# Kernel tuning notes

Measured on AMD Instinct MI355X. Metric: run time of the kernel, lower is better.

Reference implementation:

```python
import jax, jax.numpy as jnp
import numpy as np

TOP_K = 2


def _mlp(x, w1, b1, w2, b2):
    # Linear -> GELU -> Linear (assumed MLP body)
    h = jax.nn.gelu(jnp.einsum('bsd,di->bsi', x, w1) + b1)
    return jnp.einsum('bsi,id->bsd', h, w2) + b2


def setup_inputs() -> dict:
    key = jax.random.key(0)
    ks = jax.random.split(key, 8)
    B, S, D, I, E = 2, 2048, 1024, 4096, 8
    s_in = 1.0 / np.sqrt(D)
    s_mid = 1.0 / np.sqrt(I)
    return {
        'x': jax.random.normal(ks[0], (B, S, D), jnp.float32),
        'gate_w': jax.random.normal(ks[1], (D, E), jnp.float32) * s_in,
        'gate_b': jnp.zeros((E,), jnp.float32),
        'sh_w1': jax.random.normal(ks[2], (D, I), jnp.float32) * s_in,
        'sh_b1': jnp.zeros((I,), jnp.float32),
        'sh_w2': jax.random.normal(ks[3], (I, D), jnp.float32) * s_mid,
        'sh_b2': jnp.zeros((D,), jnp.float32),
        'ew1': jax.random.normal(ks[4], (E, D, I), jnp.float32) * s_in,
        'eb1': jnp.zeros((E, I), jnp.float32),
        'ew2': jax.random.normal(ks[5], (E, I, D), jnp.float32) * s_mid,
        'eb2': jnp.zeros((E, D), jnp.float32),
    }


def reference(x, gate_w, gate_b, sh_w1, sh_b1, sh_w2, sh_b2, ew1, eb1, ew2, eb2):
    E = ew1.shape[0]
    # Router
    router_probs = jax.nn.softmax(jnp.einsum('bsd,de->bse', x, gate_w) + gate_b, axis=-1)
    expert_values, expert_indices = jax.lax.top_k(router_probs, k=TOP_K)  # (B,S,K)
    expert_values = expert_values / (jnp.sum(expert_values, axis=-1, keepdims=True) + 1e-9)
    # Dense compute of all experts (faithful to original)
    h = jax.nn.gelu(jnp.einsum('bsd,edi->bsei', x, ew1) + eb1)  # (B,S,E,I)
    all_outputs = jnp.einsum('bsei,eid->bsed', h, ew2) + eb2    # (B,S,E,D)
    # Combine: scatter top-k weights to dense (B,S,E) then weighted sum
    one_hot = jax.nn.one_hot(expert_indices, E, dtype=x.dtype)  # (B,S,K,E)
    weights_E = (one_hot * expert_values[..., None]).sum(axis=2)  # (B,S,E)
    moe_out = jnp.einsum('bse,bsed->bsd', weights_E, all_outputs)
    return x + _mlp(x, sh_w1, sh_b1, sh_w2, sh_b2) + moe_out
```

## Files before the change

kernel.cpp:

```cpp
#include <hip/hip_runtime.h>
#include <hip/hip_bf16.h>
#include <stdint.h>

typedef short bf16x8 __attribute__((ext_vector_type(8)));
typedef float f32x4  __attribute__((ext_vector_type(4)));
typedef unsigned short u16;

#define T_TOK 4096
#define D_DIM 1024
#define I_DIM 4096
#define NE    9
#define BK    32

__device__ __forceinline__ u16 f2bf(float f) {
    union { float f; uint32_t u; } v; v.f = f;
    uint32_t u = v.u;
    u += 0x7FFFu + ((u >> 16) & 1u);
    return (u16)(u >> 16);
}

__device__ __forceinline__ float gelu_fast(float v) {
    float c2 = 1.5957691216057308f * (v + 0.044715f * v * v * v);
    return v / (1.0f + __expf(-c2));
}

__device__ __forceinline__ void gl16(const void* g, void* l) {
    __builtin_amdgcn_global_load_lds(
        (const __attribute__((address_space(1))) void*)g,
        (__attribute__((address_space(3))) void*)l, 16, 0, 0);
}

#define DSR(dst, adr, IMM) \
    asm volatile("ds_read_b128 %0, %1 offset:" #IMM : "=v"(dst) : "v"(adr) : "memory")
#define WAIT_VM(N)   asm volatile("s_waitcnt vmcnt(" #N ")" ::: "memory")
#define WAIT_LG(N)   asm volatile("s_waitcnt lgkmcnt(" #N ")" ::: "memory")

__global__ void k_init(int* counts) {
    int i = threadIdx.x;
    if (i < 16) counts[i] = (i == 8) ? T_TOK : 0;
}

__global__ __launch_bounds__(256) void k_router(
    const float* __restrict__ x, const float* __restrict__ gw,
    const float* __restrict__ gb,
    int* counts, int* lists, int* tok_e, int* tok_pos, float* tok_w,
    u16* __restrict__ xb)
{
    int wave = threadIdx.x >> 6, lane = threadIdx.x & 63;
    int t = blockIdx.x * 4 + wave;
    const float* xr = x + (size_t)t * D_DIM;
    u16* xbr = xb + (size_t)t * D_DIM;

    float a[8];
#pragma unroll
    for (int e = 0; e < 8; ++e) a[e] = 0.f;
#pragma unroll
    for (int j = 0; j < D_DIM / 64; ++j) {
        int d = lane + 64 * j;
        float xv = xr[d];
        xbr[d] = f2bf(xv);
        const float4* g = (const float4*)(gw + (size_t)d * 8);
        float4 g0 = g[0], g1 = g[1];
        a[0] += xv * g0.x; a[1] += xv * g0.y; a[2] += xv * g0.z; a[3] += xv * g0.w;
        a[4] += xv * g1.x; a[5] += xv * g1.y; a[6] += xv * g1.z; a[7] += xv * g1.w;
    }
#pragma unroll
    for (int off = 32; off >= 1; off >>= 1)
#pragma unroll
        for (int e = 0; e < 8; ++e) a[e] += __shfl_xor(a[e], off);

    float l[8];
#pragma unroll
    for (int e = 0; e < 8; ++e) l[e] = a[e] + gb[e];
    float mx = l[0];
#pragma unroll
    for (int e = 1; e < 8; ++e) mx = fmaxf(mx, l[e]);
    float p[8], Z = 0.f;
#pragma unroll
    for (int e = 0; e < 8; ++e) { p[e] = expf(l[e] - mx); Z += p[e]; }
#pragma unroll
    for (int e = 0; e < 8; ++e) p[e] /= Z;

    int e0 = 0; float v0 = p[0];
#pragma unroll
    for (int e = 1; e < 8; ++e) if (p[e] > v0) { v0 = p[e]; e0 = e; }
    int e1 = -1; float v1 = -1.f;
#pragma unroll
    for (int e = 0; e < 8; ++e) if (e != e0 && p[e] > v1) { v1 = p[e]; e1 = e; }
    float denom = v0 + v1 + 1e-9f;
    float w0 = v0 / denom, w1 = v1 / denom;

    if (lane == 0) {
        int p0 = atomicAdd(&counts[e0], 1);
        int p1 = atomicAdd(&counts[e1], 1);
        lists[e0 * T_TOK + p0] = t;
        lists[e1 * T_TOK + p1] = t;
        tok_e[2 * t] = e0;  tok_e[2 * t + 1] = e1;
        tok_pos[2 * t] = p0; tok_pos[2 * t + 1] = p1;
        tok_w[2 * t] = w0;  tok_w[2 * t + 1] = w1;
    }
}

__global__ void k_prefix(const int* counts, int* offsets) {
    if (threadIdx.x == 0) {
        int o = 0;
        for (int e = 0; e < NE; ++e) { offsets[e] = o; o += counts[e]; }
        offsets[NE] = o;
    }
}

__global__ __launch_bounds__(256) void k_transcast(
    const float* __restrict__ src, u16* __restrict__ dst, int K, int N)
{
    src += (size_t)blockIdx.z * K * N;
    dst += (size_t)blockIdx.z * N * K;
    __shared__ float ls[64][33];
    int t = threadIdx.x;
    int k0 = blockIdx.y * 64, n0 = blockIdx.x * 32;
    {
        int kr = t >> 2, ng = (t & 3) * 8;
        const float* s = src + (size_t)(k0 + kr) * N + n0 + ng;
        float4 v0 = *(const float4*)s, v1 = *(const float4*)(s + 4);
        ls[kr][ng + 0] = v0.x; ls[kr][ng + 1] = v0.y; ls[kr][ng + 2] = v0.z; ls[kr][ng + 3] = v0.w;
        ls[kr][ng + 4] = v1.x; ls[kr][ng + 5] = v1.y; ls[kr][ng + 6] = v1.z; ls[kr][ng + 7] = v1.w;
    }
    __syncthreads();
    int n = t >> 3, kg = (t & 7) * 8;
    u16 o[8];
#pragma unroll
    for (int j = 0; j < 8; ++j) o[j] = f2bf(ls[kg + j][n]);
    *(bf16x8*)&dst[(size_t)(n0 + n) * K + k0 + kg] = *(bf16x8*)o;
}

template <int GEMM>
__global__ __launch_bounds__(256, 3)
void k_gemm(const u16* __restrict__ A, const u16* __restrict__ Bt,
            const float* __restrict__ be, const float* __restrict__ bsh,
            const int* __restrict__ counts, const int* __restrict__ offsets,
            const int* __restrict__ lists, void* __restrict__ Cg)
{
    constexpr int K  = (GEMM == 1) ? D_DIM : I_DIM;
    constexpr int N  = (GEMM == 1) ? I_DIM : D_DIM;
    constexpr int NT = N / 128;
    constexpr int nk = K / BK;

    const int bid = blockIdx.x;
    const int g  = ((bid >> 3) >> 5) * 8 + (bid & 7);
    const int mt = (bid >> 3) & 31;
    const int e  = g / NT, nt = g % NT;
    const int cnt = counts[e];
    if (mt * 128 >= cnt) return;
    const int off = offsets[e];

    __shared__ __align__(16) u16 As0[4096], As1[4096], As2[4096];
    __shared__ __align__(16) u16 Bs0[4096], Bs1[4096], Bs2[4096];

    const int tid = threadIdx.x, w = tid >> 6, l = tid & 63;
    const int wu = __builtin_amdgcn_readfirstlane(w);
    const int wr = w >> 1, wc = w & 1;

    const int scol = ((l & 3) ^ ((l >> 3) & 3)) * 8;
    const uint32_t rch  = (uint32_t)(((l >> 4) ^ (((l & 15) >> 1) & 3)) << 4);
    const uint32_t aoff = (uint32_t)((wr * 64 + (l & 15)) * 64) + rch;
    const uint32_t boff = (uint32_t)((wc * 64 + (l & 15)) * 64) + rch;
    const uint32_t adr_a0 = (uint32_t)(uintptr_t)As0 + aoff;
    const uint32_t adr_a1 = (uint32_t)(uintptr_t)As1 + aoff;
    const uint32_t adr_a2 = (uint32_t)(uintptr_t)As2 + aoff;
    const uint32_t adr_b0 = (uint32_t)(uintptr_t)Bs0 + boff;
    const uint32_t adr_b1 = (uint32_t)(uintptr_t)Bs1 + boff;
    const uint32_t adr_b2 = (uint32_t)(uintptr_t)Bs2 + boff;

    const u16* Be = Bt + (size_t)e * N * K;
    const u16* aptr[2];
    const u16* bptr[2];
#pragma unroll
    for (int q = 0; q < 2; ++q) {
        int row = mt * 128 + w * 32 + q * 16 + (l >> 2);
        int srow;
        if constexpr (GEMM == 1) {
            if (e == 8) srow = row;
            else        srow = lists[e * T_TOK + (row < cnt ? row : cnt - 1)];
        } else {
            srow = off + row;
        }
        aptr[q] = A + (size_t)srow * K + scol;
        bptr[q] = Be + (size_t)(nt * 128 + w * 32 + q * 16 + (l >> 2)) * K + scol;
    }

    f32x4 zero = {0.f, 0.f, 0.f, 0.f};
    f32x4 acc[4][4];
#pragma unroll
    for (int m = 0; m < 4; ++m)
#pragma unroll
        for (int n = 0; n < 4; ++n) acc[m][n] = zero;

    auto STG = [&](u16* Asb, u16* Bsb, int kt) {
        const int ko = kt * BK;
#pragma unroll
        for (int q = 0; q < 2; ++q) {
            gl16(aptr[q] + ko, Asb + wu * 1024 + q * 512);
            gl16(bptr[q] + ko, Bsb + wu * 1024 + q * 512);
        }
    };
    auto RDM = [&](uint32_t aA, uint32_t aB, bool st, u16* sA, u16* sB, int knext) {
        bf16x8 fa[4], fb[4];
        DSR(fa[0], aA, 0);    DSR(fa[1], aA, 1024);
        DSR(fa[2], aA, 2048); DSR(fa[3], aA, 3072);
        DSR(fb[0], aB, 0);    DSR(fb[1], aB, 1024);
        DSR(fb[2], aB, 2048); DSR(fb[3], aB, 3072);
        WAIT_LG(0);
        __builtin_amdgcn_sched_barrier(0);
        __builtin_amdgcn_s_barrier();
        if (st) STG(sA, sB, knext);
        __builtin_amdgcn_s_setprio(1);
#pragma unroll
        for (int m = 0; m < 4; ++m)
#pragma unroll
            for (int n = 0; n < 4; ++n)
                acc[m][n] = __builtin_amdgcn_mfma_f32_16x16x32_bf16(fa[m], fb[n], acc[m][n], 0, 0, 0);
        __builtin_amdgcn_s_setprio(0);
    };

    STG(As0, Bs0, 0);
    STG(As1, Bs1, 1);
    STG(As2, Bs2, 2);
    for (int b = 0; b + 5 < nk; b += 3) {
        WAIT_VM(8); __builtin_amdgcn_s_barrier();
        RDM(adr_a0, adr_b0, true, As0, Bs0, b + 3);
        WAIT_VM(8); __builtin_amdgcn_s_barrier();
        RDM(adr_a1, adr_b1, true, As1, Bs1, b + 4);
        WAIT_VM(8); __builtin_amdgcn_s_barrier();
        RDM(adr_a2, adr_b2, true, As2, Bs2, b + 5);
    }
    WAIT_VM(8); __builtin_amdgcn_s_barrier();
    RDM(adr_a0, adr_b0, true, As0, Bs0, nk - 2);
    WAIT_VM(8); __builtin_amdgcn_s_barrier();
    RDM(adr_a1, adr_b1, true, As1, Bs1, nk - 1);
    WAIT_VM(8); __builtin_amdgcn_s_barrier();
    RDM(adr_a2, adr_b2, false, As2, Bs2, 0);
    WAIT_VM(4); __builtin_amdgcn_s_barrier();
    RDM(adr_a0, adr_b0, false, As0, Bs0, 0);
    WAIT_VM(0); __builtin_amdgcn_s_barrier();
    RDM(adr_a1, adr_b1, false, As1, Bs1, 0);

    const float* bias = (e == 8) ? bsh : (be + (size_t)e * N);
#pragma unroll
    for (int m = 0; m < 4; ++m) {
        int pbase = mt * 128 + wr * 64 + m * 16 + (l >> 4) * 4;
#pragma unroll
        for (int n = 0; n < 4; ++n) {
            int gcol = nt * 128 + wc * 64 + n * 16 + (l & 15);
            float bv = bias[gcol];
#pragma unroll
            for (int r = 0; r < 4; ++r) {
                int pos = pbase + r;
                if (pos < cnt) {
                    float v = acc[m][n][r] + bv;
                    if constexpr (GEMM == 1)
                        ((u16*)Cg)[(size_t)(off + pos) * N + gcol] = f2bf(gelu_fast(v));
                    else
                        ((float*)Cg)[(size_t)(off + pos) * N + gcol] = v;
                }
            }
        }
    }
}

__global__ __launch_bounds__(256) void k_combine(
    const float* __restrict__ x, const float* __restrict__ P,
    const int* __restrict__ offsets, const int* __restrict__ tok_e,
    const int* __restrict__ tok_pos, const float* __restrict__ tok_w,
    float* __restrict__ out)
{
    int t = blockIdx.x;
    int e0 = tok_e[2 * t], e1 = tok_e[2 * t + 1];
    int r0 = offsets[e0] + tok_pos[2 * t];
    int r1 = offsets[e1] + tok_pos[2 * t + 1];
    int rs = offsets[8] + t;
    float w0 = tok_w[2 * t], w1 = tok_w[2 * t + 1];
    int i = threadIdx.x * 4;

    float4 xv = *(const float4*)(x + (size_t)t * D_DIM + i);
    float4 ps = *(const float4*)(P + (size_t)rs * D_DIM + i);
    float4 p0 = *(const float4*)(P + (size_t)r0 * D_DIM + i);
    float4 p1 = *(const float4*)(P + (size_t)r1 * D_DIM + i);
    float4 o;
    o.x = xv.x + ps.x + w0 * p0.x + w1 * p1.x;
    o.y = xv.y + ps.y + w0 * p0.y + w1 * p1.y;
    o.z = xv.z + ps.z + w0 * p0.z + w1 * p1.z;
    o.w = xv.w + ps.w + w0 * p0.w + w1 * p1.w;
    *(float4*)(out + (size_t)t * D_DIM + i) = o;
}

extern "C" void kernel_launch(void* const* d_in, const int* in_sizes, int n_in,
                              void* d_out, int out_size, void* d_ws, size_t ws_size,
                              hipStream_t stream)
{
    const float* x   = (const float*)d_in[0];
    const float* gw  = (const float*)d_in[1];
    const float* gb  = (const float*)d_in[2];
    const float* sw1 = (const float*)d_in[3];
    const float* sb1 = (const float*)d_in[4];
    const float* sw2 = (const float*)d_in[5];
    const float* sb2 = (const float*)d_in[6];
    const float* ew1 = (const float*)d_in[7];
    const float* eb1 = (const float*)d_in[8];
    const float* ew2 = (const float*)d_in[9];
    const float* eb2 = (const float*)d_in[10];

    char* w = (char*)d_ws;
    int* counts  = (int*)w;
    int* offsets = (int*)(w + 64);
    int* tok_e   = (int*)(w + 2048);
    int* tok_pos = tok_e + 2 * T_TOK;
    float* tok_w = (float*)(tok_pos + 2 * T_TOK);
    int* lists   = (int*)(tok_w + 2 * T_TOK);

    size_t o = (size_t)1 << 20;
    u16* xb  = (u16*)(w + o);
    o += (size_t)T_TOK * D_DIM * 2;
    u16* H   = (u16*)(w + o);
    o += (size_t)3 * T_TOK * I_DIM * 2;
    u16* Wt  = (u16*)(w + o);
    o += (size_t)NE * I_DIM * D_DIM * 2;
    float* P = (float*)(w + o);

    k_init<<<1, 64, 0, stream>>>(counts);

    k_transcast<<<dim3(I_DIM / 32, D_DIM / 64, 8), 256, 0, stream>>>(ew1, Wt, D_DIM, I_DIM);
    k_transcast<<<dim3(I_DIM / 32, D_DIM / 64, 1), 256, 0, stream>>>(
        sw1, Wt + (size_t)8 * I_DIM * D_DIM, D_DIM, I_DIM);

    k_router<<<T_TOK / 4, 256, 0, stream>>>(x, gw, gb, counts, lists, tok_e, tok_pos, tok_w, xb);
    k_prefix<<<1, 64, 0, stream>>>(counts, offsets);

    k_gemm<1><<<NE * (I_DIM / 128) * 32, 256, 0, stream>>>(
        xb, Wt, eb1, sb1, counts, offsets, lists, (void*)H);

    k_transcast<<<dim3(D_DIM / 32, I_DIM / 64, 8), 256, 0, stream>>>(ew2, Wt, I_DIM, D_DIM);
    k_transcast<<<dim3(D_DIM / 32, I_DIM / 64, 1), 256, 0, stream>>>(
        sw2, Wt + (size_t)8 * I_DIM * D_DIM, I_DIM, D_DIM);

    k_gemm<2><<<NE * (D_DIM / 128) * 32, 256, 0, stream>>>(
        H, Wt, eb2, sb2, counts, offsets, lists, (void*)P);

    k_combine<<<T_TOK, 256, 0, stream>>>(x, P, offsets, tok_e, tok_pos, tok_w, (float*)d_out);
}
```

Measured before the change: 573.7 us.

## Compact grouped-GEMM work list to skip empty expert tiles

The prefix kernel now builds a compact list of (expert, m-tile) pairs for non-empty tiles, and both grouped GEMMs map blocks onto that list instead of a dense expert×32 m-tile grid. The grid is sized by a MAXPAIRS bound of 104, and blocks beyond the actual work count exit early. The aim is to avoid launching many blocks that return immediately and to spread the real work evenly across the 8-way XCD interleave. It relies on the pair count staying at or below MAXPAIRS, which holds for 8 experts with top-2 routing plus the shared expert.

```diff
diff --git a/kernel.cpp b/kernel.cpp
--- a/kernel.cpp
+++ b/kernel.cpp
@@ -11,6 +11,7 @@
 #define I_DIM 4096
 #define NE    9
 #define BK    32
+#define MAXPAIRS 104
 
 __device__ __forceinline__ u16 f2bf(float f) {
     union { float f; uint32_t u; } v; v.f = f;
@@ -101,11 +102,17 @@
     }
 }
 
-__global__ void k_prefix(const int* counts, int* offsets) {
+__global__ void k_prefix(const int* counts, int* offsets, int* pairs, int* nwork) {
     if (threadIdx.x == 0) {
-        int o = 0;
-        for (int e = 0; e < NE; ++e) { offsets[e] = o; o += counts[e]; }
+        int o = 0, np = 0;
+        for (int e = 0; e < NE; ++e) {
+            offsets[e] = o;
+            int ntile = (counts[e] + 127) >> 7;
+            for (int m = 0; m < ntile; ++m) pairs[np++] = (e << 8) | m;
+            o += counts[e];
+        }
         offsets[NE] = o;
+        nwork[0] = np;
     }
 }
 
@@ -137,19 +144,26 @@
 void k_gemm(const u16* __restrict__ A, const u16* __restrict__ Bt,
             const float* __restrict__ be, const float* __restrict__ bsh,
             const int* __restrict__ counts, const int* __restrict__ offsets,
-            const int* __restrict__ lists, void* __restrict__ Cg)
+            const int* __restrict__ lists, const int* __restrict__ pairs,
+            const int* __restrict__ nwork, void* __restrict__ Cg)
 {
     constexpr int K  = (GEMM == 1) ? D_DIM : I_DIM;
     constexpr int N  = (GEMM == 1) ? I_DIM : D_DIM;
     constexpr int NT = N / 128;
     constexpr int nk = K / BK;
 
-    const int bid = blockIdx.x;
-    const int g  = ((bid >> 3) >> 5) * 8 + (bid & 7);
-    const int mt = (bid >> 3) & 31;
-    const int e  = g / NT, nt = g % NT;
+    const int npairs = nwork[0];
+    const int W   = npairs * NT;
+    const int CPX = (W + 7) >> 3;
+    const int slot = blockIdx.x >> 3;
+    if (slot >= CPX) return;
+    const int item = (blockIdx.x & 7) * CPX + slot;
+    if (item >= W) return;
+    const int nt = item / npairs;
+    const int pi = item - nt * npairs;
+    const int pe = pairs[pi];
+    const int e = pe >> 8, mt = pe & 255;
     const int cnt = counts[e];
-    if (mt * 128 >= cnt) return;
     const int off = offsets[e];
 
     __shared__ __align__(16) u16 As0[4096], As1[4096], As2[4096];
@@ -311,6 +325,8 @@
     char* w = (char*)d_ws;
     int* counts  = (int*)w;
     int* offsets = (int*)(w + 64);
+    int* nwork   = (int*)(w + 128);
+    int* pairs   = (int*)(w + 192);
     int* tok_e   = (int*)(w + 2048);
     int* tok_pos = tok_e + 2 * T_TOK;
     float* tok_w = (float*)(tok_pos + 2 * T_TOK);
@@ -332,17 +348,17 @@
         sw1, Wt + (size_t)8 * I_DIM * D_DIM, D_DIM, I_DIM);
 
     k_router<<<T_TOK / 4, 256, 0, stream>>>(x, gw, gb, counts, lists, tok_e, tok_pos, tok_w, xb);
-    k_prefix<<<1, 64, 0, stream>>>(counts, offsets);
-
-    k_gemm<1><<<NE * (I_DIM / 128) * 32, 256, 0, stream>>>(
-        xb, Wt, eb1, sb1, counts, offsets, lists, (void*)H);
+    k_prefix<<<1, 64, 0, stream>>>(counts, offsets, pairs, nwork);
+
+    k_gemm<1><<<8 * ((MAXPAIRS * (I_DIM / 128) + 7) / 8), 256, 0, stream>>>(
+        xb, Wt, eb1, sb1, counts, offsets, lists, pairs, nwork, (void*)H);
 
     k_transcast<<<dim3(D_DIM / 32, I_DIM / 64, 8), 256, 0, stream>>>(ew2, Wt, I_DIM, D_DIM);
     k_transcast<<<dim3(D_DIM / 32, I_DIM / 64, 1), 256, 0, stream>>>(
         sw2, Wt + (size_t)8 * I_DIM * D_DIM, I_DIM, D_DIM);
 
-    k_gemm<2><<<NE * (D_DIM / 128) * 32, 256, 0, stream>>>(
-        H, Wt, eb2, sb2, counts, offsets, lists, (void*)P);
+    k_gemm<2><<<8 * ((MAXPAIRS * (D_DIM / 128) + 7) / 8), 256, 0, stream>>>(
+        H, Wt, eb2, sb2, counts, offsets, lists, pairs, nwork, (void*)P);
 
     k_combine<<<T_TOK, 256, 0, stream>>>(x, P, offsets, tok_e, tok_pos, tok_w, (float*)d_out);
 }
```

After: 583.8 us. About the same (+1.8%).
